# Kernel tuning notes

Measured on AMD Instinct MI355X. Metric: run time of the kernel, lower is better.

## Reference

```python
import jax, jax.numpy as jnp
import numpy as np

B, S, D_IN = 2, 2048, 1024
H, DA, DH = 16, 64, 64          # num_heads, attention_dim, head_dim (linear_hidden_dim)
EMBED = 1024
KSIZE = 1


def causal_conv1d(x_bsc, w):
    """x_bsc: (B,S,Cin); w: (Cout,Cin,K). Left-pad K-1 -> causal. Returns (B,Cout,S)."""
    k = w.shape[-1]
    x_bcs = jnp.transpose(x_bsc, (0, 2, 1))
    x_bcs = jnp.pad(x_bcs, ((0, 0), (0, 0), (k - 1, 0)))
    return jax.lax.conv_general_dilated(
        x_bcs, w, window_strides=(1,), padding='VALID',
        dimension_numbers=('NCH', 'OIH', 'NCH'))


def setup_inputs() -> dict:
    key = jax.random.key(0)
    ks = jax.random.split(key, 7)
    x = jax.random.normal(ks[0], (B, S, D_IN), dtype=jnp.float32)
    # causal mask: 1 where attended, 0 where masked (masked_fill where ==0)
    attn_mask = jnp.tril(jnp.ones((S, S), dtype=jnp.int32))[None, None]  # (1,1,S,S)
    wq = 0.02 * jax.random.normal(ks[1], (H * DA, D_IN, KSIZE), dtype=jnp.float32)
    wk = 0.02 * jax.random.normal(ks[2], (H * DA, D_IN, KSIZE), dtype=jnp.float32)
    wv = 0.02 * jax.random.normal(ks[3], (H * DH, D_IN, KSIZE), dtype=jnp.float32)
    w_out = 0.02 * jax.random.normal(ks[4], (EMBED, H * DH), dtype=jnp.float32)
    b_out = 0.02 * jax.random.normal(ks[5], (EMBED,), dtype=jnp.float32)
    return {"x": x, "attn_mask": attn_mask, "wq": wq, "wk": wk, "wv": wv,
            "w_out": w_out, "b_out": b_out}


def reference(x, attn_mask, wq, wk, wv, w_out, b_out):
    b, s, _ = x.shape
    scale = DH ** (-0.5)  # NOTE: torch code scales by head_dim, not attention_dim
    q = causal_conv1d(x, wq)  # (B, H*DA, S)
    k = causal_conv1d(x, wk)  # (B, H*DA, S)
    v = causal_conv1d(x, wv)  # (B, H*DH, S)
    q = q.reshape(b, H, DA, s).transpose(0, 1, 3, 2)  # (B,H,S,DA)
    k = k.reshape(b, H, DA, s).transpose(0, 1, 3, 2)
    v = v.reshape(b, H, DH, s).transpose(0, 1, 3, 2)  # (B,H,S,DH)
    scores = scale * jnp.einsum('bhnd,bhmd->bhnm', q, k)
    scores = jnp.where(attn_mask == 0, -jnp.inf, scores)
    probs = jax.nn.softmax(scores, axis=-1)
    context = jnp.einsum('bhnm,bhmd->bhnd', probs, v)  # (B,H,S,DH)
    context = context.transpose(0, 2, 1, 3).reshape(b, s, H * DH)
    return context @ w_out.T + b_out
```

## Files before the change

kernel.cpp:

```cpp
#include <hip/hip_runtime.h>
#include <math.h>


typedef __bf16 bf16;
typedef __bf16 bf16x8 __attribute__((ext_vector_type(8)));
typedef __bf16 bf16x4 __attribute__((ext_vector_type(4)));
typedef float  f32x4  __attribute__((ext_vector_type(4)));

#define MFMA16(a, b, c) __builtin_amdgcn_mfma_f32_16x16x32_bf16((a), (b), (c), 0, 0, 0)

__device__ __forceinline__ void gll16(const void* g, void* l) {
    __builtin_amdgcn_global_load_lds(
        (__attribute__((address_space(1))) unsigned int*)g,
        (__attribute__((address_space(3))) unsigned int*)l, 16, 0, 0);
}

__global__ __launch_bounds__(256) void cvt_all_kernel(
    const float* __restrict__ x,  const float* __restrict__ wq,
    const float* __restrict__ wk, const float* __restrict__ wv,
    const float* __restrict__ wo,
    bf16* __restrict__ xb,  bf16* __restrict__ wqb, bf16* __restrict__ wkb,
    bf16* __restrict__ wvb, bf16* __restrict__ wob)
{
    const int blk = blockIdx.x;
    const float* src; bf16* dst; int off; float scale = 1.f;
    if (blk < 4096)      { src = x;  dst = xb;  off = blk * 1024; }
    else if (blk < 5120) { src = wq; dst = wqb; off = (blk - 4096) * 1024;
                           scale = 0.18033688011112042f; }
    else if (blk < 6144) { src = wk; dst = wkb; off = (blk - 5120) * 1024; }
    else if (blk < 7168) { src = wv; dst = wvb; off = (blk - 6144) * 1024; }
    else                 { src = wo; dst = wob; off = (blk - 7168) * 1024; }
    const int i = off + threadIdx.x * 4;
    f32x4 v = *(const f32x4*)(src + i);
    bf16x4 o;
    o[0] = (bf16)(v[0] * scale); o[1] = (bf16)(v[1] * scale);
    o[2] = (bf16)(v[2] * scale); o[3] = (bf16)(v[3] * scale);
    *(bf16x4*)(dst + i) = o;
}

__global__ __launch_bounds__(256, 3) void qkv_mfma_kernel(
    const bf16* __restrict__ xb, const bf16* __restrict__ wqb,
    const bf16* __restrict__ wkb, const bf16* __restrict__ wvb,
    bf16* __restrict__ Qb, bf16* __restrict__ Kb, bf16* __restrict__ Vtb)
{
    __shared__ bf16 As[2][128 * 32];
    __shared__ bf16 Bs[2][128 * 32];
    const int mt = blockIdx.x;
    const int nt = blockIdx.y;
    const int which = nt >> 3;
    const bf16* Wm = (which == 0) ? wqb : (which == 1) ? wkb : wvb;

    const int t = threadIdx.x;
    const int w = t >> 6, lane = t & 63, quad = lane >> 4, l16 = lane & 15;
    const int wm = (w >> 1) * 64, wn = (w & 1) * 64;
    const int srow = lane >> 2;
    const int scol = (lane & 3) * 8;

    const bf16* Ab = xb + ((size_t)(mt * 128) + srow) * 1024 + scol;
    const bf16* Bb = Wm + ((size_t)((nt & 7) * 128) + srow) * 1024 + scol;

    f32x4 acc[4][4];
    #pragma unroll
    for (int i = 0; i < 4; i++)
        #pragma unroll
        for (int j = 0; j < 4; j++)
            #pragma unroll
            for (int r = 0; r < 4; r++) acc[i][j][r] = 0.f;

    gll16(Ab + (size_t)(w * 16) * 1024,       As[0] + w * 512);
    gll16(Ab + (size_t)((w + 4) * 16) * 1024, As[0] + (w + 4) * 512);
    gll16(Bb + (size_t)(w * 16) * 1024,       Bs[0] + w * 512);
    gll16(Bb + (size_t)((w + 4) * 16) * 1024, Bs[0] + (w + 4) * 512);

    for (int it = 0; it < 32; it++) {
        const int cur = it & 1, nxt = cur ^ 1;
        __syncthreads();
        if (it < 31) {
            const int kn = it * 32 + 32;
            gll16(Ab + (size_t)(w * 16) * 1024 + kn,       As[nxt] + w * 512);
            gll16(Ab + (size_t)((w + 4) * 16) * 1024 + kn, As[nxt] + (w + 4) * 512);
            gll16(Bb + (size_t)(w * 16) * 1024 + kn,       Bs[nxt] + w * 512);
            gll16(Bb + (size_t)((w + 4) * 16) * 1024 + kn, Bs[nxt] + (w + 4) * 512);
        }
        bf16x8 af[4], bfr[4];
        #pragma unroll
        for (int i = 0; i < 4; i++)
            af[i] = *(const bf16x8*)&As[cur][(wm + i * 16 + l16) * 32 + quad * 8];
        #pragma unroll
        for (int j = 0; j < 4; j++)
            bfr[j] = *(const bf16x8*)&Bs[cur][(wn + j * 16 + l16) * 32 + quad * 8];
        #pragma unroll
        for (int i = 0; i < 4; i++)
            #pragma unroll
            for (int j = 0; j < 4; j++)
                acc[i][j] = MFMA16(af[i], bfr[j], acc[i][j]);
    }

    const int nbase = (nt & 7) * 128 + wn;
    if (which == 2) {
        #pragma unroll
        for (int i = 0; i < 4; i++) {
            const int m0 = mt * 128 + wm + i * 16 + quad * 4;
            const int bb = m0 >> 11, s0 = m0 & 2047;
            #pragma unroll
            for (int j = 0; j < 4; j++) {
                const int n = nbase + j * 16 + l16;
                const int h = n >> 6, d = n & 63;
                bf16x4 pk;
                #pragma unroll
                for (int r = 0; r < 4; r++) pk[r] = (bf16)acc[i][j][r];
                *(bf16x4*)&Vtb[(((size_t)(bb * 16 + h)) * 64 + d) * 2048 + s0] = pk;
            }
        }
    } else {
        bf16* Out = (which == 0) ? Qb : Kb;
        #pragma unroll
        for (int i = 0; i < 4; i++) {
            #pragma unroll
            for (int r = 0; r < 4; r++) {
                const int m = mt * 128 + wm + i * 16 + quad * 4 + r;
                const int bb = m >> 11, s = m & 2047;
                #pragma unroll
                for (int j = 0; j < 4; j++) {
                    const int n = nbase + j * 16 + l16;
                    const int h = n >> 6, d = n & 63;
                    Out[(((size_t)(bb * 16 + h)) * 2048 + s) * 64 + d] =
                        (bf16)acc[i][j][r];
                }
            }
        }
    }
}

__global__ __launch_bounds__(256, 2) void attn_mfma_kernel(
    const bf16* __restrict__ Qb, const bf16* __restrict__ Kb,
    const bf16* __restrict__ Vtb, bf16* __restrict__ ctxb)
{
    __shared__ bf16 Ks[2][64 * 64];
    __shared__ bf16 Vts[2][64 * 64];
    __shared__ bf16 Pl[4][16 * 64];

    const int id = blockIdx.x;
    const int bh = id & 31;
    const int pr = id >> 5;
    const int qa = pr, qb = 31 - pr;
    const int h = bh & 15, b = bh >> 4;
    const int t = threadIdx.x;
    const int w = t >> 6, lane = t & 63, quad = lane >> 4, l16 = lane & 15;
    const int e8 = l16 & 7;
    const int sr = lane >> 3, sc = lane & 7;

    const size_t hb = (size_t)(b * 16 + h);
    const bf16* Qh = Qb + hb * (2048 * 64);
    const bf16* Kh = Kb + hb * (2048 * 64);
    const bf16* Vh = Vtb + hb * (64 * 2048);

    bf16x8 qf0[2], qf1[2];
    {
        const bf16* Qr0 = Qh + (size_t)(qa * 64 + w * 16 + l16) * 64;
        qf0[0] = *(const bf16x8*)(Qr0 + quad * 8);
        qf0[1] = *(const bf16x8*)(Qr0 + 32 + quad * 8);
        const bf16* Qr1 = Qh + (size_t)(qb * 64 + w * 16 + l16) * 64;
        qf1[0] = *(const bf16x8*)(Qr1 + quad * 8);
        qf1[1] = *(const bf16x8*)(Qr1 + 32 + quad * 8);
    }

    bf16x8 ones;
    #pragma unroll
    for (int i = 0; i < 8; i++) ones[i] = (bf16)1.0f;

    f32x4 o0[4], o1[4], l0, l1;
    #pragma unroll
    for (int r = 0; r < 4; r++) { l0[r] = 0.f; l1[r] = 0.f; }
    #pragma unroll
    for (int dt = 0; dt < 4; dt++)
        #pragma unroll
        for (int r = 0; r < 4; r++) { o0[dt][r] = 0.f; o1[dt][r] = 0.f; }

    #define STAGE(ktv, buf)                                                   \
        {                                                                     \
            const int r0 = w * 8 + sr, r1 = (w + 4) * 8 + sr;                 \
            gll16(Kh + (size_t)((ktv) * 64 + r0) * 64 + (sc ^ sr) * 8,        \
                  Ks[buf] + w * 512);                                         \
            gll16(Kh + (size_t)((ktv) * 64 + r1) * 64 + (sc ^ sr) * 8,        \
                  Ks[buf] + (w + 4) * 512);                                   \
            gll16(Vh + (size_t)r0 * 2048 + (ktv) * 64 + (sc ^ sr) * 8,        \
                  Vts[buf] + w * 512);                                        \
            gll16(Vh + (size_t)r1 * 2048 + (ktv) * 64 + (sc ^ sr) * 8,        \
                  Vts[buf] + (w + 4) * 512);                                  \
        }

    #define ITER(qt64, ktv, diag, qfv, oacc, lacc, cur)                       \
        {                                                                     \
            f32x4 sacc[4];                                                    \
            _Pragma("unroll")                                                 \
            for (int tt = 0; tt < 4; tt++) {                                  \
                _Pragma("unroll")                                             \
                for (int r = 0; r < 4; r++) sacc[tt][r] = 0.f;                \
            }                                                                 \
            _Pragma("unroll")                                                 \
            for (int tt = 0; tt < 4; tt++) {                                  \
                const int krow = tt * 16 + l16;                               \
                bf16x8 kf0 = *(const bf16x8*)&Ks[cur][krow * 64 +             \
                                   ((quad)     ^ (krow & 7)) * 8];            \
                bf16x8 kf1 = *(const bf16x8*)&Ks[cur][krow * 64 +             \
                                   ((quad + 4) ^ (krow & 7)) * 8];            \
                sacc[tt] = MFMA16(kf0, (qfv)[0], sacc[tt]);                   \
                sacc[tt] = MFMA16(kf1, (qfv)[1], sacc[tt]);                   \
            }                                                                 \
            const int qrow = (qt64) * 64 + w * 16 + l16;                      \
            _Pragma("unroll")                                                 \
            for (int tt = 0; tt < 4; tt++) {                                  \
                bf16x4 pk;                                                    \
                _Pragma("unroll")                                             \
                for (int r = 0; r < 4; r++) {                                 \
                    float p = __builtin_amdgcn_exp2f(sacc[tt][r]);            \
                    if ((diag) && ((ktv) * 64 + tt * 16 + quad * 4 + r) > qrow) \
                        p = 0.f;                                              \
                    pk[r] = (bf16)p;                                          \
                }                                                             \
                const int cs = (tt * 2 + (quad >> 1)) ^ e8;                   \
                *(bf16x4*)&Pl[w][l16 * 64 + cs * 8 + (quad & 1) * 4] = pk;    \
            }                                                                 \
            bf16x8 ap0 = *(const bf16x8*)&Pl[w][l16 * 64 + ((quad) ^ e8) * 8];\
            bf16x8 ap1 = *(const bf16x8*)&Pl[w][l16 * 64 +                    \
                                                (((quad + 4)) ^ e8) * 8];     \
            (lacc) = MFMA16(ap0, ones, (lacc));                               \
            (lacc) = MFMA16(ap1, ones, (lacc));                               \
            _Pragma("unroll")                                                 \
            for (int dt = 0; dt < 4; dt++) {                                  \
                const int drow = dt * 16 + l16;                               \
                bf16x8 bv0 = *(const bf16x8*)&Vts[cur][drow * 64 +            \
                                   ((quad)     ^ (drow & 7)) * 8];            \
                bf16x8 bv1 = *(const bf16x8*)&Vts[cur][drow * 64 +            \
                                   ((quad + 4) ^ (drow & 7)) * 8];            \
                (oacc)[dt] = MFMA16(ap0, bv0, (oacc)[dt]);                    \
                (oacc)[dt] = MFMA16(ap1, bv1, (oacc)[dt]);                    \
            }                                                                 \
        }

    STAGE(0, 0);

    const int a = qa;
    for (int vkt = 0; vkt < 33; vkt++) {
        const int cur = vkt & 1, nxt = cur ^ 1;
        __syncthreads();
        if (vkt < 32) {
            const int vn = vkt + 1;
            const int ktn = (vn <= a) ? vn : vn - (a + 1);
            STAGE(ktn, nxt);
        }
        if (vkt <= a) {
            ITER(qa, vkt, (vkt == a), qf0, o0, l0, cur);
        } else {
            const int kt = vkt - (a + 1);
            ITER(qb, kt, (vkt == 32), qf1, o1, l1, cur);
        }
    }
    #undef STAGE
    #undef ITER

    #pragma unroll
    for (int r = 0; r < 4; r++) {
        const float inv0 = 1.f / l0[r];
        const int s0 = qa * 64 + w * 16 + quad * 4 + r;
        const float inv1 = 1.f / l1[r];
        const int s1 = qb * 64 + w * 16 + quad * 4 + r;
        #pragma unroll
        for (int dt = 0; dt < 4; dt++) {
            ctxb[((size_t)(b * 2048 + s0)) * 1024 + h * 64 + dt * 16 + l16] =
                (bf16)(o0[dt][r] * inv0);
            ctxb[((size_t)(b * 2048 + s1)) * 1024 + h * 64 + dt * 16 + l16] =
                (bf16)(o1[dt][r] * inv1);
        }
    }
}

__global__ __launch_bounds__(256, 2) void oproj_mfma_kernel(
    const bf16* __restrict__ ctxb, const bf16* __restrict__ wob,
    const float* __restrict__ b_out, float* __restrict__ out)
{
    __shared__ bf16 As[2][64 * 32];
    __shared__ bf16 Bs[2][128 * 32];
    const int mt = blockIdx.x;
    const int nt = blockIdx.y;
    const int t = threadIdx.x;
    const int w = t >> 6, lane = t & 63, quad = lane >> 4, l16 = lane & 15;
    const int srow = lane >> 2;
    const int scol = (lane & 3) * 8;

    const bf16* Ab = ctxb + (size_t)(mt * 64 + srow) * 1024 + scol;
    const bf16* Bb = wob + (size_t)(nt * 128 + srow) * 1024 + scol;

    f32x4 acc[8];
    #pragma unroll
    for (int j = 0; j < 8; j++)
        #pragma unroll
        for (int r = 0; r < 4; r++) acc[j][r] = 0.f;

    gll16(Ab + (size_t)(w * 16) * 1024,       As[0] + w * 512);
    gll16(Bb + (size_t)(w * 16) * 1024,       Bs[0] + w * 512);
    gll16(Bb + (size_t)((w + 4) * 16) * 1024, Bs[0] + (w + 4) * 512);

    for (int it = 0; it < 32; it++) {
        const int cur = it & 1, nxt = cur ^ 1;
        __syncthreads();
        if (it < 31) {
            const int kn = it * 32 + 32;
            gll16(Ab + (size_t)(w * 16) * 1024 + kn,       As[nxt] + w * 512);
            gll16(Bb + (size_t)(w * 16) * 1024 + kn,       Bs[nxt] + w * 512);
            gll16(Bb + (size_t)((w + 4) * 16) * 1024 + kn, Bs[nxt] + (w + 4) * 512);
        }
        bf16x8 af = *(const bf16x8*)&As[cur][(w * 16 + l16) * 32 + quad * 8];
        #pragma unroll
        for (int j = 0; j < 8; j++) {
            bf16x8 bfr = *(const bf16x8*)&Bs[cur][(j * 16 + l16) * 32 + quad * 8];
            acc[j] = MFMA16(af, bfr, acc[j]);
        }
    }

    #pragma unroll
    for (int j = 0; j < 8; j++)
        #pragma unroll
        for (int r = 0; r < 4; r++) {
            const int m = mt * 64 + w * 16 + quad * 4 + r;
            const int n = nt * 128 + j * 16 + l16;
            out[(size_t)m * 1024 + n] = acc[j][r] + b_out[n];
        }
}

extern "C" void kernel_launch(void* const* d_in, const int* in_sizes, int n_in,
                              void* d_out, int out_size, void* d_ws, size_t ws_size,
                              hipStream_t stream)
{
    const float* x     = (const float*)d_in[0];
    const float* wq    = (const float*)d_in[2];
    const float* wk    = (const float*)d_in[3];
    const float* wv    = (const float*)d_in[4];
    const float* w_out = (const float*)d_in[5];
    const float* b_out = (const float*)d_in[6];
    float* out = (float*)d_out;

    char* ws = (char*)d_ws;
    bf16* xb   = (bf16*)(ws);
    bf16* wqb  = (bf16*)(ws + (8u  << 20));
    bf16* wkb  = (bf16*)(ws + (10u << 20));
    bf16* wvb  = (bf16*)(ws + (12u << 20));
    bf16* wob  = (bf16*)(ws + (14u << 20));
    bf16* Qb   = (bf16*)(ws + (16u << 20));
    bf16* Kb   = (bf16*)(ws + (24u << 20));
    bf16* Vtb  = (bf16*)(ws + (32u << 20));
    bf16* ctxb = (bf16*)(ws + (40u << 20));

    cvt_all_kernel<<<8192, 256, 0, stream>>>(x, wq, wk, wv, w_out,
                                             xb, wqb, wkb, wvb, wob);
    qkv_mfma_kernel<<<dim3(32, 24), 256, 0, stream>>>(xb, wqb, wkb, wvb, Qb, Kb, Vtb);
    attn_mfma_kernel<<<512, 256, 0, stream>>>(Qb, Kb, Vtb, ctxb);
    oproj_mfma_kernel<<<dim3(64, 8), 256, 0, stream>>>(ctxb, wob, b_out, out);
}
```

Before: 193.0 us.

## Halve attention block to two waves, each handling two query row tiles

The attention kernel now launches 128 threads (2 waves) per block instead of 256, and each wave processes 32 query rows as two 16-row sub-tiles. K and V fragments are loaded from LDS once per key tile and reused across both sub-tiles, which halves LDS fragment reads per query row. Each wave also issues more staging loads. The cost is higher register pressure from doubled accumulators and fewer waves per block to hide latency, which could lower occupancy.

```diff
diff --git a/kernel.cpp b/kernel.cpp
--- a/kernel.cpp
+++ b/kernel.cpp
@@ -132,7 +132,7 @@
     }
 }
 
-__global__ __launch_bounds__(256, 2) void attn_mfma_kernel(
+__global__ __launch_bounds__(128, 2) void attn_mfma_kernel(
     const bf16* __restrict__ Qb, const bf16* __restrict__ Kb,
     const bf16* __restrict__ Vtb, bf16* __restrict__ ctxb)
 {
@@ -146,7 +146,8 @@
     const int qa = pr, qb = 31 - pr;
     const int h = bh & 15, b = bh >> 4;
     const int t = threadIdx.x;
-    const int w = t >> 6, lane = t & 63, quad = lane >> 4, l16 = lane & 15;
+    const int w = t >> 6;
+    const int lane = t & 63, quad = lane >> 4, l16 = lane & 15;
     const int e8 = l16 & 7;
     const int sr = lane >> 3, sc = lane & 7;
 
@@ -155,87 +156,98 @@
     const bf16* Kh = Kb + hb * (2048 * 64);
     const bf16* Vh = Vtb + hb * (64 * 2048);
 
-    bf16x8 qf0[2], qf1[2];
-    {
-        const bf16* Qr0 = Qh + (size_t)(qa * 64 + w * 16 + l16) * 64;
-        qf0[0] = *(const bf16x8*)(Qr0 + quad * 8);
-        qf0[1] = *(const bf16x8*)(Qr0 + 32 + quad * 8);
-        const bf16* Qr1 = Qh + (size_t)(qb * 64 + w * 16 + l16) * 64;
-        qf1[0] = *(const bf16x8*)(Qr1 + quad * 8);
-        qf1[1] = *(const bf16x8*)(Qr1 + 32 + quad * 8);
+    bf16x8 qf0[2][2], qf1[2][2];
+    #pragma unroll
+    for (int rt = 0; rt < 2; rt++) {
+        const bf16* Qr0 = Qh + (size_t)(qa * 64 + w * 32 + rt * 16 + l16) * 64;
+        qf0[rt][0] = *(const bf16x8*)(Qr0 + quad * 8);
+        qf0[rt][1] = *(const bf16x8*)(Qr0 + 32 + quad * 8);
+        const bf16* Qr1 = Qh + (size_t)(qb * 64 + w * 32 + rt * 16 + l16) * 64;
+        qf1[rt][0] = *(const bf16x8*)(Qr1 + quad * 8);
+        qf1[rt][1] = *(const bf16x8*)(Qr1 + 32 + quad * 8);
     }
 
     bf16x8 ones;
     #pragma unroll
     for (int i = 0; i < 8; i++) ones[i] = (bf16)1.0f;
 
-    f32x4 o0[4], o1[4], l0, l1;
-    #pragma unroll
-    for (int r = 0; r < 4; r++) { l0[r] = 0.f; l1[r] = 0.f; }
-    #pragma unroll
-    for (int dt = 0; dt < 4; dt++)
-        #pragma unroll
-        for (int r = 0; r < 4; r++) { o0[dt][r] = 0.f; o1[dt][r] = 0.f; }
+    f32x4 o0[2][4], o1[2][4], l0[2], l1[2];
+    #pragma unroll
+    for (int rt = 0; rt < 2; rt++) {
+        #pragma unroll
+        for (int r = 0; r < 4; r++) { l0[rt][r] = 0.f; l1[rt][r] = 0.f; }
+        #pragma unroll
+        for (int dt = 0; dt < 4; dt++)
+            #pragma unroll
+            for (int r = 0; r < 4; r++) { o0[rt][dt][r] = 0.f; o1[rt][dt][r] = 0.f; }
+    }
 
     #define STAGE(ktv, buf)                                                   \
         {                                                                     \
-            const int r0 = w * 8 + sr, r1 = (w + 4) * 8 + sr;                 \
-            gll16(Kh + (size_t)((ktv) * 64 + r0) * 64 + (sc ^ sr) * 8,        \
-                  Ks[buf] + w * 512);                                         \
-            gll16(Kh + (size_t)((ktv) * 64 + r1) * 64 + (sc ^ sr) * 8,        \
-                  Ks[buf] + (w + 4) * 512);                                   \
-            gll16(Vh + (size_t)r0 * 2048 + (ktv) * 64 + (sc ^ sr) * 8,        \
-                  Vts[buf] + w * 512);                                        \
-            gll16(Vh + (size_t)r1 * 2048 + (ktv) * 64 + (sc ^ sr) * 8,        \
-                  Vts[buf] + (w + 4) * 512);                                  \
+            _Pragma("unroll")                                                 \
+            for (int j = 0; j < 4; j++) {                                     \
+                const int c = 4 * w + j;                                      \
+                const int r = c * 8 + sr;                                     \
+                gll16(Kh + (size_t)((ktv) * 64 + r) * 64 + (sc ^ sr) * 8,     \
+                      Ks[buf] + c * 512);                                     \
+                gll16(Vh + (size_t)r * 2048 + (ktv) * 64 + (sc ^ sr) * 8,     \
+                      Vts[buf] + c * 512);                                    \
+            }                                                                 \
         }
 
     #define ITER(qt64, ktv, diag, qfv, oacc, lacc, cur)                       \
         {                                                                     \
-            f32x4 sacc[4];                                                    \
-            _Pragma("unroll")                                                 \
-            for (int tt = 0; tt < 4; tt++) {                                  \
-                _Pragma("unroll")                                             \
-                for (int r = 0; r < 4; r++) sacc[tt][r] = 0.f;                \
-            }                                                                 \
+            bf16x8 kf[4][2], bv[4][2];                                        \
             _Pragma("unroll")                                                 \
             for (int tt = 0; tt < 4; tt++) {                                  \
                 const int krow = tt * 16 + l16;                               \
-                bf16x8 kf0 = *(const bf16x8*)&Ks[cur][krow * 64 +             \
-                                   ((quad)     ^ (krow & 7)) * 8];            \
-                bf16x8 kf1 = *(const bf16x8*)&Ks[cur][krow * 64 +             \
-                                   ((quad + 4) ^ (krow & 7)) * 8];            \
-                sacc[tt] = MFMA16(kf0, (qfv)[0], sacc[tt]);                   \
-                sacc[tt] = MFMA16(kf1, (qfv)[1], sacc[tt]);                   \
+                kf[tt][0] = *(const bf16x8*)&Ks[cur][krow * 64 +              \
+                                 ((quad)     ^ (krow & 7)) * 8];              \
+                kf[tt][1] = *(const bf16x8*)&Ks[cur][krow * 64 +              \
+                                 ((quad + 4) ^ (krow & 7)) * 8];              \
             }                                                                 \
-            const int qrow = (qt64) * 64 + w * 16 + l16;                      \
-            _Pragma("unroll")                                                 \
-            for (int tt = 0; tt < 4; tt++) {                                  \
-                bf16x4 pk;                                                    \
-                _Pragma("unroll")                                             \
-                for (int r = 0; r < 4; r++) {                                 \
-                    float p = __builtin_amdgcn_exp2f(sacc[tt][r]);            \
-                    if ((diag) && ((ktv) * 64 + tt * 16 + quad * 4 + r) > qrow) \
-                        p = 0.f;                                              \
-                    pk[r] = (bf16)p;                                          \
-                }                                                             \
-                const int cs = (tt * 2 + (quad >> 1)) ^ e8;                   \
-                *(bf16x4*)&Pl[w][l16 * 64 + cs * 8 + (quad & 1) * 4] = pk;    \
-            }                                                                 \
-            bf16x8 ap0 = *(const bf16x8*)&Pl[w][l16 * 64 + ((quad) ^ e8) * 8];\
-            bf16x8 ap1 = *(const bf16x8*)&Pl[w][l16 * 64 +                    \
-                                                (((quad + 4)) ^ e8) * 8];     \
-            (lacc) = MFMA16(ap0, ones, (lacc));                               \
-            (lacc) = MFMA16(ap1, ones, (lacc));                               \
             _Pragma("unroll")                                                 \
             for (int dt = 0; dt < 4; dt++) {                                  \
                 const int drow = dt * 16 + l16;                               \
-                bf16x8 bv0 = *(const bf16x8*)&Vts[cur][drow * 64 +            \
-                                   ((quad)     ^ (drow & 7)) * 8];            \
-                bf16x8 bv1 = *(const bf16x8*)&Vts[cur][drow * 64 +            \
-                                   ((quad + 4) ^ (drow & 7)) * 8];            \
-                (oacc)[dt] = MFMA16(ap0, bv0, (oacc)[dt]);                    \
-                (oacc)[dt] = MFMA16(ap1, bv1, (oacc)[dt]);                    \
+                bv[dt][0] = *(const bf16x8*)&Vts[cur][drow * 64 +             \
+                                 ((quad)     ^ (drow & 7)) * 8];              \
+                bv[dt][1] = *(const bf16x8*)&Vts[cur][drow * 64 +             \
+                                 ((quad + 4) ^ (drow & 7)) * 8];              \
+            }                                                                 \
+            _Pragma("unroll")                                                 \
+            for (int rt = 0; rt < 2; rt++) {                                  \
+                f32x4 sacc[4];                                                \
+                _Pragma("unroll")                                             \
+                for (int tt = 0; tt < 4; tt++) {                              \
+                    _Pragma("unroll")                                         \
+                    for (int r = 0; r < 4; r++) sacc[tt][r] = 0.f;            \
+                    sacc[tt] = MFMA16(kf[tt][0], (qfv)[rt][0], sacc[tt]);     \
+                    sacc[tt] = MFMA16(kf[tt][1], (qfv)[rt][1], sacc[tt]);     \
+                }                                                             \
+                const int qrow = (qt64) * 64 + w * 32 + rt * 16 + l16;        \
+                bf16* Prt = &Pl[w * 2 + rt][0];                               \
+                _Pragma("unroll")                                             \
+                for (int tt = 0; tt < 4; tt++) {                              \
+                    bf16x4 pk;                                                \
+                    _Pragma("unroll")                                         \
+                    for (int r = 0; r < 4; r++) {                             \
+                        float p = __builtin_amdgcn_exp2f(sacc[tt][r]);        \
+                        if ((diag) && ((ktv) * 64 + tt * 16 + quad * 4 + r) > qrow) \
+                            p = 0.f;                                          \
+                        pk[r] = (bf16)p;                                      \
+                    }                                                         \
+                    const int cs = (tt * 2 + (quad >> 1)) ^ e8;               \
+                    *(bf16x4*)&Prt[l16 * 64 + cs * 8 + (quad & 1) * 4] = pk;  \
+                }                                                             \
+                bf16x8 ap0 = *(const bf16x8*)&Prt[l16 * 64 + ((quad) ^ e8) * 8];   \
+                bf16x8 ap1 = *(const bf16x8*)&Prt[l16 * 64 + ((quad + 4) ^ e8) * 8];\
+                (lacc)[rt] = MFMA16(ap0, ones, (lacc)[rt]);                   \
+                (lacc)[rt] = MFMA16(ap1, ones, (lacc)[rt]);                   \
+                _Pragma("unroll")                                             \
+                for (int dt = 0; dt < 4; dt++) {                              \
+                    (oacc)[rt][dt] = MFMA16(ap0, bv[dt][0], (oacc)[rt][dt]);  \
+                    (oacc)[rt][dt] = MFMA16(ap1, bv[dt][1], (oacc)[rt][dt]);  \
+                }                                                             \
             }                                                                 \
         }
 
@@ -261,19 +273,21 @@
     #undef ITER
 
     #pragma unroll
-    for (int r = 0; r < 4; r++) {
-        const float inv0 = 1.f / l0[r];
-        const int s0 = qa * 64 + w * 16 + quad * 4 + r;
-        const float inv1 = 1.f / l1[r];
-        const int s1 = qb * 64 + w * 16 + quad * 4 + r;
-        #pragma unroll
-        for (int dt = 0; dt < 4; dt++) {
-            ctxb[((size_t)(b * 2048 + s0)) * 1024 + h * 64 + dt * 16 + l16] =
-                (bf16)(o0[dt][r] * inv0);
-            ctxb[((size_t)(b * 2048 + s1)) * 1024 + h * 64 + dt * 16 + l16] =
-                (bf16)(o1[dt][r] * inv1);
-        }
-    }
+    for (int rt = 0; rt < 2; rt++)
+        #pragma unroll
+        for (int r = 0; r < 4; r++) {
+            const float inv0 = 1.f / l0[rt][r];
+            const int s0 = qa * 64 + w * 32 + rt * 16 + quad * 4 + r;
+            const float inv1 = 1.f / l1[rt][r];
+            const int s1 = qb * 64 + w * 32 + rt * 16 + quad * 4 + r;
+            #pragma unroll
+            for (int dt = 0; dt < 4; dt++) {
+                ctxb[((size_t)(b * 2048 + s0)) * 1024 + h * 64 + dt * 16 + l16] =
+                    (bf16)(o0[rt][dt][r] * inv0);
+                ctxb[((size_t)(b * 2048 + s1)) * 1024 + h * 64 + dt * 16 + l16] =
+                    (bf16)(o1[rt][dt][r] * inv1);
+            }
+        }
 }
 
 __global__ __launch_bounds__(256, 2) void oproj_mfma_kernel(
@@ -355,6 +369,6 @@
     cvt_all_kernel<<<8192, 256, 0, stream>>>(x, wq, wk, wv, w_out,
                                              xb, wqb, wkb, wvb, wob);
     qkv_mfma_kernel<<<dim3(32, 24), 256, 0, stream>>>(xb, wqb, wkb, wvb, Qb, Kb, Vtb);
-    attn_mfma_kernel<<<512, 256, 0, stream>>>(Qb, Kb, Vtb, ctxb);
+    attn_mfma_kernel<<<512, 128, 0, stream>>>(Qb, Kb, Vtb, ctxb);
     oproj_mfma_kernel<<<dim3(64, 8), 256, 0, stream>>>(ctxb, wob, b_out, out);
 }
```

Result: slower. 204.5 us (+6.0%).
